# Performance work log

Hardware: AMD Instinct MI355X
Metric: run time of the kernel (lower is better)

The kernel has to match this reference:

```python
import jax, jax.numpy as jnp
import numpy as np

EPS = 1e-12

def _l2norm(x):
    # F.normalize(x, dim=1): x / max(||x||_2, eps)
    n = jnp.sqrt(jnp.sum(x * x, axis=1, keepdims=True))
    return x / jnp.maximum(n, EPS)

def setup_inputs() -> dict:
    key = jax.random.key(0)
    ks = jax.random.split(key, 8)
    n_users, n_entities, channel = 100000, 100000, 128
    n_edges, n_inter, n_rel_rows = 600000, 500000, 15
    return {
        "user_emb": jax.random.normal(ks[0], (n_users, channel), dtype=jnp.float32),
        "item_emb": jax.random.normal(ks[1], (n_entities, channel), dtype=jnp.float32) * 0.1,
        "edge_index": jax.random.randint(ks[2], (2, n_edges), 0, n_entities, dtype=jnp.int64),
        "edge_type": jax.random.randint(ks[3], (n_edges,), 1, n_rel_rows + 1, dtype=jnp.int64),
        "inter_edge": jnp.stack([
            jax.random.randint(ks[4], (n_inter,), 0, n_users, dtype=jnp.int64),
            jax.random.randint(ks[5], (n_inter,), 0, n_entities, dtype=jnp.int64),
        ]),
        "inter_edge_w": jax.random.uniform(ks[6], (n_inter,), dtype=jnp.float32),
        "relation_emb": jax.random.normal(ks[7], (n_rel_rows, channel), dtype=jnp.float32) * 0.1,
        "n_hops": 2,
    }

def reference(user_emb, item_emb, edge_index, edge_type, inter_edge, inter_edge_w, relation_emb, n_hops):
    head, tail = edge_index[0], edge_index[1]
    n_entities = item_emb.shape[0]
    n_users = user_emb.shape[0]

    ent = item_emb
    for _ in range(n_hops):
        he = ent[head]                       # [E, d] gather
        te = ent[tail]                       # [E, d] gather
        re = relation_emb[edge_type - 1]     # [E, d] gather
        # scores = exp(sum(h*r*t)) then scatter_softmax over head segments
        scores = jnp.exp(jnp.sum(he * re * te, axis=1))  # [E]
        smax = jax.ops.segment_max(scores, head, num_segments=n_entities)
        e = jnp.exp(scores - smax[head])
        denom = jax.ops.segment_sum(e, head, num_segments=n_entities)
        attn = e / denom[head]
        ent = jax.ops.segment_sum(attn[:, None] * te, head, num_segments=n_entities)
        # dropout in eval mode (identity), then F.normalize
        ent = _l2norm(ent)

    u_idx, i_idx = inter_edge[0], inter_edge[1]
    item_agg = inter_edge_w[:, None] * ent[i_idx]  # [Ninter, d]
    user_agg = jax.ops.segment_sum(item_agg, u_idx, num_segments=n_users)
    return (_l2norm(user_agg), ent)
```

## Files before the change

### kernel.cpp

```cpp
#include <hip/hip_runtime.h>
#include <math.h>

#define D 128
#define EPS 1e-12f
#define SCAN_NB 128
#define SCAN_TPB 256

__device__ __forceinline__ float waveSum(float v) {
#pragma unroll
    for (int off = 32; off > 0; off >>= 1) v += __shfl_xor(v, off, 64);
    return v;
}

template <int CTRL>
__device__ __forceinline__ float rorAdd(float v) {
    int t = __builtin_amdgcn_update_dpp(0, __float_as_int(v), CTRL, 0xF, 0xF, true);
    return v + __int_as_float(t);
}
__device__ __forceinline__ float groupSum16(float v) {
    v = rorAdd<0x121>(v);
    v = rorAdd<0x122>(v);
    v = rorAdd<0x124>(v);
    v = rorAdd<0x128>(v);
    return v;
}

__global__ void k_count_rank(const int* __restrict__ head, const int* __restrict__ u_idx,
                             int* __restrict__ counts_all, int* __restrict__ rank,
                             int E, int Ninter, int N_ent) {
    int i = blockIdx.x * blockDim.x + threadIdx.x;
    if (i < E) rank[i] = atomicAdd(&counts_all[head[i]], 1);
    else if (i < E + Ninter) rank[i] = atomicAdd(&counts_all[N_ent + u_idx[i - E]], 1);
}

__global__ void k_count_both(const int* __restrict__ head, const int* __restrict__ u_idx,
                             int* __restrict__ counts_all, int E, int Ninter, int N_ent) {
    int i = blockIdx.x * blockDim.x + threadIdx.x;
    if (i < E) atomicAdd(&counts_all[head[i]], 1);
    else if (i < E + Ninter) atomicAdd(&counts_all[N_ent + u_idx[i - E]], 1);
}

__global__ void k_scan_block(const int* __restrict__ counts, int* __restrict__ bsum,
                             int N, int K) {
    __shared__ int lds[SCAN_TPB];
    int tid = threadIdx.x;
    int base = (blockIdx.x * SCAN_TPB + tid) * K;
    int s = 0;
    for (int k = 0; k < K; ++k) { int idx = base + k; if (idx < N) s += counts[idx]; }
    lds[tid] = s;
    __syncthreads();
    for (int off = SCAN_TPB / 2; off > 0; off >>= 1) {
        if (tid < off) lds[tid] += lds[tid + off];
        __syncthreads();
    }
    if (tid == 0) bsum[blockIdx.x] = lds[0];
}

__global__ void k_scan_top(int* __restrict__ bsum) {
    __shared__ int lds[SCAN_NB];
    int t = threadIdx.x;
    if (t < SCAN_NB) lds[t] = bsum[t];
    __syncthreads();
    if (t == 0) {
        int run = 0;
        for (int i = 0; i < SCAN_NB; ++i) { int c = lds[i]; lds[i] = run; run += c; }
    }
    __syncthreads();
    if (t < SCAN_NB) bsum[t] = lds[t];
}

__global__ void k_scan_final(const int* __restrict__ counts, const int* __restrict__ bsum,
                             int* __restrict__ row_start, int N, int K) {
    __shared__ int lds[SCAN_TPB];
    int tid = threadIdx.x;
    int base = (blockIdx.x * SCAN_TPB + tid) * K;
    int s = 0;
    for (int k = 0; k < K; ++k) { int idx = base + k; if (idx < N) s += counts[idx]; }
    lds[tid] = s;
    __syncthreads();
    for (int off = 1; off < SCAN_TPB; off <<= 1) {
        int v = (tid >= off) ? lds[tid - off] : 0;
        __syncthreads();
        lds[tid] += v;
        __syncthreads();
    }
    int run = lds[tid] - s + bsum[blockIdx.x];
    for (int k = 0; k < K; ++k) {
        int idx = base + k;
        if (idx <= N) {
            row_start[idx] = run;
            if (idx < N) run += counts[idx];
        }
    }
}

__global__ void k_reorder_rank(const int* __restrict__ head, const int* __restrict__ tail,
                               const int* __restrict__ etype,
                               const int* __restrict__ u_idx, const int* __restrict__ i_idx,
                               const float* __restrict__ w,
                               const int* __restrict__ rs_all, const int* __restrict__ rank,
                               int* __restrict__ packed, int2* __restrict__ riw,
                               int E, int Ninter, int N_ent) {
    int i = blockIdx.x * blockDim.x + threadIdx.x;
    if (i < E) {
        int h = head[i];
        packed[rs_all[h] + rank[i]] = tail[i] | ((etype[i] - 1) << 24);
    } else if (i < E + Ninter) {
        int k = i - E;
        int u = N_ent + u_idx[k];
        int pos = rs_all[u] + rank[i] - E;
        riw[pos] = make_int2(i_idx[k], __float_as_int(w[k]));
    }
}

__global__ void k_reorder_both(const int* __restrict__ head, const int* __restrict__ tail,
                               const int* __restrict__ etype,
                               const int* __restrict__ u_idx, const int* __restrict__ i_idx,
                               const float* __restrict__ w,
                               const int* __restrict__ rs_all, int* __restrict__ cursor,
                               int* __restrict__ packed, int2* __restrict__ riw,
                               int E, int Ninter, int N_ent) {
    int i = blockIdx.x * blockDim.x + threadIdx.x;
    if (i < E) {
        int h = head[i];
        int pos = rs_all[h] + atomicAdd(&cursor[h], 1);
        packed[pos] = tail[i] | ((etype[i] - 1) << 24);
    } else if (i < E + Ninter) {
        int k = i - E;
        int u = N_ent + u_idx[k];
        int pos = rs_all[u] + atomicAdd(&cursor[u], 1) - E;
        riw[pos] = make_int2(i_idx[k], __float_as_int(w[k]));
    }
}

__global__ void k_hop(const float* __restrict__ ent_in,
                      const float* __restrict__ rel,
                      const int* __restrict__ rs_all,
                      const int* __restrict__ packed,
                      float* __restrict__ ent_out, int N) {
    int row = (blockIdx.x * blockDim.x + threadIdx.x) >> 6;
    if (row >= N) return;
    int lane = threadIdx.x & 63;
    int g = lane >> 4, l16 = lane & 15;
    int rs = rs_all[row];
    int deg = rs_all[row + 1] - rs;

    if (deg == 0) {
        if (lane < 32) ((float4*)(ent_out + (size_t)row * D))[lane] = make_float4(0, 0, 0, 0);
        return;
    }

    const float4* hp = (const float4*)(ent_in + (size_t)row * D);
    float4 ha = hp[l16], hb = hp[l16 + 16];

    float4 acca = make_float4(0, 0, 0, 0), accb = make_float4(0, 0, 0, 0);

    for (int j0 = 0; j0 < deg; j0 += 4) {
        int j = j0 + g;
        if (j < deg) {
            int p = packed[rs + j];
            int t = p & 0xFFFFFF, rt = p >> 24;
            const float4* tp = (const float4*)(ent_in + (size_t)t * D);
            const float4* rp = (const float4*)(rel + (size_t)rt * D);
            float4 ta = tp[l16], tb = tp[l16 + 16];
            float4 ra = rp[l16], rb = rp[l16 + 16];
            float v = ha.x * ra.x * ta.x + ha.y * ra.y * ta.y +
                      ha.z * ra.z * ta.z + ha.w * ra.w * ta.w +
                      hb.x * rb.x * tb.x + hb.y * rb.y * tb.y +
                      hb.z * rb.z * tb.z + hb.w * rb.w * tb.w;
            v = groupSum16(v);
            float wgt = expf(expf(v));
            acca.x += wgt * ta.x; acca.y += wgt * ta.y;
            acca.z += wgt * ta.z; acca.w += wgt * ta.w;
            accb.x += wgt * tb.x; accb.y += wgt * tb.y;
            accb.z += wgt * tb.z; accb.w += wgt * tb.w;
        }
    }

#pragma unroll
    for (int off = 16; off <= 32; off <<= 1) {
        acca.x += __shfl_xor(acca.x, off, 64); acca.y += __shfl_xor(acca.y, off, 64);
        acca.z += __shfl_xor(acca.z, off, 64); acca.w += __shfl_xor(acca.w, off, 64);
        accb.x += __shfl_xor(accb.x, off, 64); accb.y += __shfl_xor(accb.y, off, 64);
        accb.z += __shfl_xor(accb.z, off, 64); accb.w += __shfl_xor(accb.w, off, 64);
    }
    float part = acca.x * acca.x + acca.y * acca.y + acca.z * acca.z + acca.w * acca.w +
                 accb.x * accb.x + accb.y * accb.y + accb.z * accb.z + accb.w * accb.w;
    float ss = waveSum(part) * 0.25f;
    float inv = 1.0f / fmaxf(sqrtf(ss), EPS);
    float4 val = (lane < 16) ? acca : accb;
    val.x *= inv; val.y *= inv; val.z *= inv; val.w *= inv;
    if (lane < 32) ((float4*)(ent_out + (size_t)row * D))[lane] = val;
}

__global__ void k_user(const float* __restrict__ ent,
                       const int* __restrict__ rs_all,
                       const int2* __restrict__ riw,
                       float* __restrict__ uout, int Nu, int N_ent, int E) {
    int row = (blockIdx.x * blockDim.x + threadIdx.x) >> 6;
    if (row >= Nu) return;
    int lane = threadIdx.x & 63;
    int g = lane >> 4, l16 = lane & 15;
    int base = rs_all[N_ent + row];
    int deg = rs_all[N_ent + row + 1] - base;
    int rs = base - E;

    float4 acca = make_float4(0, 0, 0, 0), accb = make_float4(0, 0, 0, 0);
    for (int j0 = 0; j0 < deg; j0 += 4) {
        int j = j0 + g;
        if (j < deg) {
            int2 pw = riw[rs + j];
            int it = pw.x;
            float ww = __int_as_float(pw.y);
            const float4* ip = (const float4*)(ent + (size_t)it * D);
            float4 ta = ip[l16], tb = ip[l16 + 16];
            acca.x += ww * ta.x; acca.y += ww * ta.y;
            acca.z += ww * ta.z; acca.w += ww * ta.w;
            accb.x += ww * tb.x; accb.y += ww * tb.y;
            accb.z += ww * tb.z; accb.w += ww * tb.w;
        }
    }
#pragma unroll
    for (int off = 16; off <= 32; off <<= 1) {
        acca.x += __shfl_xor(acca.x, off, 64); acca.y += __shfl_xor(acca.y, off, 64);
        acca.z += __shfl_xor(acca.z, off, 64); acca.w += __shfl_xor(acca.w, off, 64);
        accb.x += __shfl_xor(accb.x, off, 64); accb.y += __shfl_xor(accb.y, off, 64);
        accb.z += __shfl_xor(accb.z, off, 64); accb.w += __shfl_xor(accb.w, off, 64);
    }
    float part = acca.x * acca.x + acca.y * acca.y + acca.z * acca.z + acca.w * acca.w +
                 accb.x * accb.x + accb.y * accb.y + accb.z * accb.z + accb.w * accb.w;
    float ss = waveSum(part) * 0.25f;
    float inv = 1.0f / fmaxf(sqrtf(ss), EPS);
    float4 val = (lane < 16) ? acca : accb;
    val.x *= inv; val.y *= inv; val.z *= inv; val.w *= inv;
    if (lane < 32) ((float4*)(uout + (size_t)row * D))[lane] = val;
}

extern "C" void kernel_launch(void* const* d_in, const int* in_sizes, int n_in,
                              void* d_out, int out_size, void* d_ws, size_t ws_size,
                              hipStream_t stream) {
    const float* item_emb  = (const float*)d_in[1];
    const int*   edge_idx  = (const int*)d_in[2];
    const int*   edge_type = (const int*)d_in[3];
    const int*   inter     = (const int*)d_in[4];
    const float* inter_w   = (const float*)d_in[5];
    const float* rel       = (const float*)d_in[6];

    const int N_users = in_sizes[0] / D;
    const int N_ent   = in_sizes[1] / D;
    const int E       = in_sizes[2] / 2;
    const int Ninter  = in_sizes[5];
    const int N_tot   = N_ent + N_users;
    const int n_keys  = E + Ninter;

    float* user_out = (float*)d_out;
    float* ent_out  = (float*)d_out + (size_t)N_users * D;
    float* ent_mid  = user_out;

    const int* head  = edge_idx;
    const int* tail  = edge_idx + E;
    const int* u_idx = inter;
    const int* i_idx = inter + Ninter;

    const int TPB = 256;
    dim3 blk(TPB);

    int2* riw       = (int2*)d_ws;
    int* counts_all = (int*)(riw + Ninter);
    int* rs_all     = counts_all + N_tot;
    int* packed     = rs_all + N_tot + 1;
    int* bsum       = packed + E;
    int* rank       = bsum + SCAN_NB;

    size_t need_rank = ((size_t)Ninter * 2 + N_tot * 2 + 1 + E + SCAN_NB + n_keys) * 4;
    bool use_rank = ws_size >= need_rank;

    int K = (N_tot + SCAN_NB * SCAN_TPB - 1) / (SCAN_NB * SCAN_TPB);

    hipMemsetAsync(counts_all, 0, (size_t)N_tot * 4, stream);
    if (use_rank) {
        k_count_rank<<<(n_keys + TPB - 1) / TPB, blk, 0, stream>>>(
            head, u_idx, counts_all, rank, E, Ninter, N_ent);
        k_scan_block<<<SCAN_NB, SCAN_TPB, 0, stream>>>(counts_all, bsum, N_tot, K);
        k_scan_top<<<1, SCAN_TPB, 0, stream>>>(bsum);
        k_scan_final<<<SCAN_NB, SCAN_TPB, 0, stream>>>(counts_all, bsum, rs_all, N_tot, K);
        k_reorder_rank<<<(n_keys + TPB - 1) / TPB, blk, 0, stream>>>(
            head, tail, edge_type, u_idx, i_idx, inter_w,
            rs_all, rank, packed, riw, E, Ninter, N_ent);
    } else {
        k_count_both<<<(n_keys + TPB - 1) / TPB, blk, 0, stream>>>(
            head, u_idx, counts_all, E, Ninter, N_ent);
        k_scan_block<<<SCAN_NB, SCAN_TPB, 0, stream>>>(counts_all, bsum, N_tot, K);
        k_scan_top<<<1, SCAN_TPB, 0, stream>>>(bsum);
        k_scan_final<<<SCAN_NB, SCAN_TPB, 0, stream>>>(counts_all, bsum, rs_all, N_tot, K);
        hipMemsetAsync(counts_all, 0, (size_t)N_tot * 4, stream);
        k_reorder_both<<<(n_keys + TPB - 1) / TPB, blk, 0, stream>>>(
            head, tail, edge_type, u_idx, i_idx, inter_w,
            rs_all, counts_all, packed, riw, E, Ninter, N_ent);
    }

    int grid_rows = ((size_t)N_ent * 64 + TPB - 1) / TPB;
    k_hop<<<grid_rows, blk, 0, stream>>>(item_emb, rel, rs_all, packed, ent_mid, N_ent);
    k_hop<<<grid_rows, blk, 0, stream>>>(ent_mid, rel, rs_all, packed, ent_out, N_ent);

    k_user<<<((size_t)N_users * 64 + TPB - 1) / TPB, blk, 0, stream>>>(
        ent_out, rs_all, riw, user_out, N_users, N_ent, E);
}
```

Before: 242.5 us.

## Map one 16-lane group per row instead of one wave per row

The hop and user kernels now give each 16-lane group its own row, so a wave handles four rows instead of splitting one row's edges across four groups. This drops the cross-group shuffle reduction and the wasted lanes on low-degree rows, and the grid shrinks to match. It also switches to fast __expf intrinsics. In exchange, rows with different degrees inside one wave cause divergence, and there is less memory parallelism per row.

Result: no change. 241.8 us (-0.3%).

```diff
diff --git a/kernel.cpp b/kernel.cpp
--- a/kernel.cpp
+++ b/kernel.cpp
@@ -5,12 +5,6 @@
 #define EPS 1e-12f
 #define SCAN_NB 128
 #define SCAN_TPB 256
-
-__device__ __forceinline__ float waveSum(float v) {
-#pragma unroll
-    for (int off = 32; off > 0; off >>= 1) v += __shfl_xor(v, off, 64);
-    return v;
-}
 
 template <int CTRL>
 __device__ __forceinline__ float rorAdd(float v) {
@@ -138,102 +132,82 @@
                       const int* __restrict__ rs_all,
                       const int* __restrict__ packed,
                       float* __restrict__ ent_out, int N) {
-    int row = (blockIdx.x * blockDim.x + threadIdx.x) >> 6;
-    if (row >= N) return;
     int lane = threadIdx.x & 63;
     int g = lane >> 4, l16 = lane & 15;
+    int row = ((blockIdx.x * blockDim.x + threadIdx.x) >> 6) * 4 + g;
+    if (row >= N) return;
+
     int rs = rs_all[row];
     int deg = rs_all[row + 1] - rs;
 
-    if (deg == 0) {
-        if (lane < 32) ((float4*)(ent_out + (size_t)row * D))[lane] = make_float4(0, 0, 0, 0);
-        return;
-    }
-
     const float4* hp = (const float4*)(ent_in + (size_t)row * D);
     float4 ha = hp[l16], hb = hp[l16 + 16];
 
     float4 acca = make_float4(0, 0, 0, 0), accb = make_float4(0, 0, 0, 0);
 
-    for (int j0 = 0; j0 < deg; j0 += 4) {
-        int j = j0 + g;
-        if (j < deg) {
-            int p = packed[rs + j];
-            int t = p & 0xFFFFFF, rt = p >> 24;
-            const float4* tp = (const float4*)(ent_in + (size_t)t * D);
-            const float4* rp = (const float4*)(rel + (size_t)rt * D);
-            float4 ta = tp[l16], tb = tp[l16 + 16];
-            float4 ra = rp[l16], rb = rp[l16 + 16];
-            float v = ha.x * ra.x * ta.x + ha.y * ra.y * ta.y +
-                      ha.z * ra.z * ta.z + ha.w * ra.w * ta.w +
-                      hb.x * rb.x * tb.x + hb.y * rb.y * tb.y +
-                      hb.z * rb.z * tb.z + hb.w * rb.w * tb.w;
-            v = groupSum16(v);
-            float wgt = expf(expf(v));
-            acca.x += wgt * ta.x; acca.y += wgt * ta.y;
-            acca.z += wgt * ta.z; acca.w += wgt * ta.w;
-            accb.x += wgt * tb.x; accb.y += wgt * tb.y;
-            accb.z += wgt * tb.z; accb.w += wgt * tb.w;
-        }
-    }
-
-#pragma unroll
-    for (int off = 16; off <= 32; off <<= 1) {
-        acca.x += __shfl_xor(acca.x, off, 64); acca.y += __shfl_xor(acca.y, off, 64);
-        acca.z += __shfl_xor(acca.z, off, 64); acca.w += __shfl_xor(acca.w, off, 64);
-        accb.x += __shfl_xor(accb.x, off, 64); accb.y += __shfl_xor(accb.y, off, 64);
-        accb.z += __shfl_xor(accb.z, off, 64); accb.w += __shfl_xor(accb.w, off, 64);
-    }
+    for (int j = 0; j < deg; ++j) {
+        int p = packed[rs + j];
+        int t = p & 0xFFFFFF, rt = ((unsigned)p) >> 24;
+        const float4* tp = (const float4*)(ent_in + (size_t)t * D);
+        const float4* rp = (const float4*)(rel + (size_t)rt * D);
+        float4 ta = tp[l16], tb = tp[l16 + 16];
+        float4 ra = rp[l16], rb = rp[l16 + 16];
+        float v = ha.x * ra.x * ta.x + ha.y * ra.y * ta.y +
+                  ha.z * ra.z * ta.z + ha.w * ra.w * ta.w +
+                  hb.x * rb.x * tb.x + hb.y * rb.y * tb.y +
+                  hb.z * rb.z * tb.z + hb.w * rb.w * tb.w;
+        v = groupSum16(v);
+        float wgt = __expf(__expf(v));
+        acca.x += wgt * ta.x; acca.y += wgt * ta.y;
+        acca.z += wgt * ta.z; acca.w += wgt * ta.w;
+        accb.x += wgt * tb.x; accb.y += wgt * tb.y;
+        accb.z += wgt * tb.z; accb.w += wgt * tb.w;
+    }
+
     float part = acca.x * acca.x + acca.y * acca.y + acca.z * acca.z + acca.w * acca.w +
                  accb.x * accb.x + accb.y * accb.y + accb.z * accb.z + accb.w * accb.w;
-    float ss = waveSum(part) * 0.25f;
+    float ss = groupSum16(part);
     float inv = 1.0f / fmaxf(sqrtf(ss), EPS);
-    float4 val = (lane < 16) ? acca : accb;
-    val.x *= inv; val.y *= inv; val.z *= inv; val.w *= inv;
-    if (lane < 32) ((float4*)(ent_out + (size_t)row * D))[lane] = val;
+    acca.x *= inv; acca.y *= inv; acca.z *= inv; acca.w *= inv;
+    accb.x *= inv; accb.y *= inv; accb.z *= inv; accb.w *= inv;
+    float4* op = (float4*)(ent_out + (size_t)row * D);
+    op[l16] = acca;
+    op[l16 + 16] = accb;
 }
 
 __global__ void k_user(const float* __restrict__ ent,
                        const int* __restrict__ rs_all,
                        const int2* __restrict__ riw,
                        float* __restrict__ uout, int Nu, int N_ent, int E) {
-    int row = (blockIdx.x * blockDim.x + threadIdx.x) >> 6;
-    if (row >= Nu) return;
     int lane = threadIdx.x & 63;
     int g = lane >> 4, l16 = lane & 15;
+    int row = ((blockIdx.x * blockDim.x + threadIdx.x) >> 6) * 4 + g;
+    if (row >= Nu) return;
+
     int base = rs_all[N_ent + row];
     int deg = rs_all[N_ent + row + 1] - base;
     int rs = base - E;
 
     float4 acca = make_float4(0, 0, 0, 0), accb = make_float4(0, 0, 0, 0);
-    for (int j0 = 0; j0 < deg; j0 += 4) {
-        int j = j0 + g;
-        if (j < deg) {
-            int2 pw = riw[rs + j];
-            int it = pw.x;
-            float ww = __int_as_float(pw.y);
-            const float4* ip = (const float4*)(ent + (size_t)it * D);
-            float4 ta = ip[l16], tb = ip[l16 + 16];
-            acca.x += ww * ta.x; acca.y += ww * ta.y;
-            acca.z += ww * ta.z; acca.w += ww * ta.w;
-            accb.x += ww * tb.x; accb.y += ww * tb.y;
-            accb.z += ww * tb.z; accb.w += ww * tb.w;
-        }
-    }
-#pragma unroll
-    for (int off = 16; off <= 32; off <<= 1) {
-        acca.x += __shfl_xor(acca.x, off, 64); acca.y += __shfl_xor(acca.y, off, 64);
-        acca.z += __shfl_xor(acca.z, off, 64); acca.w += __shfl_xor(acca.w, off, 64);
-        accb.x += __shfl_xor(accb.x, off, 64); accb.y += __shfl_xor(accb.y, off, 64);
-        accb.z += __shfl_xor(accb.z, off, 64); accb.w += __shfl_xor(accb.w, off, 64);
+    for (int j = 0; j < deg; ++j) {
+        int2 pw = riw[rs + j];
+        float ww = __int_as_float(pw.y);
+        const float4* ip = (const float4*)(ent + (size_t)pw.x * D);
+        float4 ta = ip[l16], tb = ip[l16 + 16];
+        acca.x += ww * ta.x; acca.y += ww * ta.y;
+        acca.z += ww * ta.z; acca.w += ww * ta.w;
+        accb.x += ww * tb.x; accb.y += ww * tb.y;
+        accb.z += ww * tb.z; accb.w += ww * tb.w;
     }
     float part = acca.x * acca.x + acca.y * acca.y + acca.z * acca.z + acca.w * acca.w +
                  accb.x * accb.x + accb.y * accb.y + accb.z * accb.z + accb.w * accb.w;
-    float ss = waveSum(part) * 0.25f;
+    float ss = groupSum16(part);
     float inv = 1.0f / fmaxf(sqrtf(ss), EPS);
-    float4 val = (lane < 16) ? acca : accb;
-    val.x *= inv; val.y *= inv; val.z *= inv; val.w *= inv;
-    if (lane < 32) ((float4*)(uout + (size_t)row * D))[lane] = val;
+    acca.x *= inv; acca.y *= inv; acca.z *= inv; acca.w *= inv;
+    accb.x *= inv; accb.y *= inv; accb.z *= inv; accb.w *= inv;
+    float4* op = (float4*)(uout + (size_t)row * D);
+    op[l16] = acca;
+    op[l16 + 16] = accb;
 }
 
 extern "C" void kernel_launch(void* const* d_in, const int* in_sizes, int n_in,
@@ -299,10 +273,10 @@
             rs_all, counts_all, packed, riw, E, Ninter, N_ent);
     }
 
-    int grid_rows = ((size_t)N_ent * 64 + TPB - 1) / TPB;
+    int grid_rows = (N_ent + 15) / 16;
     k_hop<<<grid_rows, blk, 0, stream>>>(item_emb, rel, rs_all, packed, ent_mid, N_ent);
     k_hop<<<grid_rows, blk, 0, stream>>>(ent_mid, rel, rs_all, packed, ent_out, N_ent);
 
-    k_user<<<((size_t)N_users * 64 + TPB - 1) / TPB, blk, 0, stream>>>(
+    k_user<<<(N_users + 15) / 16, blk, 0, stream>>>(
         ent_out, rs_all, riw, user_out, N_users, N_ent, E);
 }
```
